# Kernel tuning notes

Hardware: AMD Instinct MI355X
Metric: run time of the kernel (lower is better)

Reference implementation:

```python
import jax, jax.numpy as jnp
import numpy as np

H = 12
DK = 64


def setup_inputs() -> dict:
    key = jax.random.key(0)
    ks = jax.random.split(key, 6)
    bs, ne, d = 32, 20, H * DK
    R = jax.random.normal(ks[0], (bs, ne, ne, d), dtype=jnp.float32)
    R_mas = jax.random.randint(ks[1], (bs, ne, ne, 1), 0, 2).astype(jnp.float32)
    WQ_w = jax.random.normal(ks[2], (DK, DK), dtype=jnp.float32) * (1.0 / np.sqrt(DK))
    WK_w = jax.random.normal(ks[3], (DK, DK), dtype=jnp.float32) * (1.0 / np.sqrt(DK))
    WV_w = jax.random.normal(ks[4], (DK, DK), dtype=jnp.float32) * (1.0 / np.sqrt(DK))
    zb = jnp.zeros((DK,), dtype=jnp.float32)
    return {"R": R, "R_mas": R_mas, "WQ_w": WQ_w, "WQ_b": zb, "WK_w": WK_w,
            "WK_b": zb, "WV_w": WV_w, "WV_b": zb}


def reference(R, R_mas, WQ_w, WQ_b, WK_w, WK_b, WV_w, WV_b):
    bs, ne, _, d = R.shape
    h, dk = H, DK
    n = ne * ne
    # (bs, h, ne, ne, dk)
    Rh = R.reshape(bs, ne, ne, h, dk).transpose(0, 3, 1, 2, 4)
    # per-head QKV linears (torch Linear: y = x @ W.T + b)
    Q = (Rh @ WQ_w.T + WQ_b).reshape(bs, h, n, dk)
    K = (Rh @ WK_w.T + WK_b).reshape(bs, h, n, dk)
    V = (Rh @ WV_w.T + WV_b).reshape(bs, h, n, dk)
    mas = R_mas.reshape(bs, 1, n)                      # (bs,1,n)
    att_mas = mas[:, :, :, None] * mas[:, :, None, :]  # (bs,1,n,n)
    alpha = jnp.einsum('bhqd,bhkd->bhqk', Q, K)        # (bs,h,n,n)
    alpha = alpha - (1.0 - att_mas) * 100000.0         # mask BEFORE scaling (faithful)
    alpha = jax.nn.softmax(alpha / jnp.sqrt(jnp.float32(dk)), axis=-1)
    R_Z = jnp.einsum('bhqk,bhkd->bhqd', alpha, V).reshape(bs, h, ne, ne, dk)
    R_Z = R_Z * R_mas.reshape(bs, 1, ne, ne, 1)
    # (bs, ne, ne, h*dk)
    return R_Z.transpose(0, 2, 3, 1, 4).reshape(bs, ne, ne, h * dk)
```

## Files before the change

### kernel.cpp

```cpp
#include <hip/hip_runtime.h>

typedef float    f32x4 __attribute__((ext_vector_type(4)));
typedef _Float16 f16x8 __attribute__((ext_vector_type(8)));
typedef _Float16 f16x4 __attribute__((ext_vector_type(4)));
typedef _Float16 f16x2 __attribute__((ext_vector_type(2)));
typedef __fp16   fp16x2_raw __attribute__((ext_vector_type(2)));

#define MFMA16 __builtin_amdgcn_mfma_f32_16x16x32_f16

__device__ __forceinline__ f16x2 pkrtz(float a, float b) {
    fp16x2_raw t = __builtin_amdgcn_cvt_pkrtz(a, b);
    union { fp16x2_raw r; f16x2 h; } u;
    u.r = t;
    return u.h;
}
#define PKRTZ pkrtz

#define NQ     400
#define DMODEL 768

#define SCL 0.18033688011112042f
#define PEN 18033.688011112043f
#define M0  8.0f

#define K_OFF    0
#define VT_OFF   51200
#define W_OFF    105472
#define PEN_OFF  130048
#define BIAS_OFF 131648
#define MKB_OFF  132416
#define SMEM_BYTES 132480

__device__ __forceinline__ f16x8 cvt8(const float* rp) {
    f32x4 u0 = *(const f32x4*)(rp);
    f32x4 u1 = *(const f32x4*)(rp + 4);
    union { f16x2 h2[4]; f16x8 v; } u;
    u.h2[0] = PKRTZ(u0[0], u0[1]);
    u.h2[1] = PKRTZ(u0[2], u0[3]);
    u.h2[2] = PKRTZ(u1[0], u1[1]);
    u.h2[3] = PKRTZ(u1[2], u1[3]);
    return u.v;
}

__device__ __forceinline__ void proj_v(char* smem, f16x8 af0, f16x8 af1,
                                       int t, int g, int q16, int csw) {
    #pragma unroll
    for (int cg = 0; cg < 4; ++cg) {
        const int col = cg * 16 + q16;
        const float bb = *(const float*)(smem + BIAS_OFF + (128 + col) * 4);
        f32x4 acc = {bb, bb, bb, bb};
        f16x8 wb0 = *(const f16x8*)(smem + W_OFF + 16384 + col * 128 + ((g * 16) ^ csw));
        f16x8 wb1 = *(const f16x8*)(smem + W_OFF + 16384 + col * 128 + ((64 + g * 16) ^ csw));
        acc = MFMA16(af0, wb0, acc, 0, 0, 0);
        acc = MFMA16(af1, wb1, acc, 0, 0, 0);
        union { f16x2 h2[2]; f16x4 v; } hv;
        hv.h2[0] = PKRTZ(acc[0], acc[1]);
        hv.h2[1] = PKRTZ(acc[2], acc[3]);
        *(f16x4*)(smem + VT_OFF + col * 848 + (t >> 1) * 64 + g * 16 + (t & 1) * 8) = hv.v;
    }
}

__device__ __forceinline__ void proj_k(char* smem, f16x8 af0, f16x8 af1,
                                       int kk, int g, int q16, int csw) {
    #pragma unroll
    for (int cg = 0; cg < 4; ++cg) {
        const int d0 = cg * 16 + 4 * g;
        f32x4 acc = *(const f32x4*)(smem + BIAS_OFF + (64 + d0) * 4);
        f16x8 wb0 = *(const f16x8*)(smem + W_OFF + 8192 + (cg * 16 + q16) * 128 + ((g * 16) ^ csw));
        f16x8 wb1 = *(const f16x8*)(smem + W_OFF + 8192 + (cg * 16 + q16) * 128 + ((64 + g * 16) ^ csw));
        acc = MFMA16(wb0, af0, acc, 0, 0, 0);
        acc = MFMA16(wb1, af1, acc, 0, 0, 0);
        union { f16x2 h2[2]; f16x4 v; } hv;
        hv.h2[0] = PKRTZ(acc[0], acc[1]);
        hv.h2[1] = PKRTZ(acc[2], acc[3]);
        const int pos2 = ((cg & 2) << 5) + g * 16 + (cg & 1) * 8;
        *(f16x4*)(smem + K_OFF + kk * 128 + (pos2 ^ csw)) = hv.v;
    }
}

__device__ __forceinline__ void proj_q(char* smem, f16x8 af0, f16x8 af1,
                                       int g, int q16, int csw, f16x8 (&qreg)[2]) {
    f32x4 qa[4];
    #pragma unroll
    for (int cg = 0; cg < 4; ++cg) {
        const int d0 = cg * 16 + 4 * g;
        f32x4 acc = *(const f32x4*)(smem + BIAS_OFF + d0 * 4);
        f16x8 wb0 = *(const f16x8*)(smem + W_OFF + (cg * 16 + q16) * 128 + ((g * 16) ^ csw));
        f16x8 wb1 = *(const f16x8*)(smem + W_OFF + (cg * 16 + q16) * 128 + ((64 + g * 16) ^ csw));
        acc = MFMA16(wb0, af0, acc, 0, 0, 0);
        acc = MFMA16(wb1, af1, acc, 0, 0, 0);
        qa[cg] = acc;
    }
    union { f16x2 h2[4]; f16x8 v; } u0, u1;
    u0.h2[0] = PKRTZ(qa[0][0], qa[0][1]);
    u0.h2[1] = PKRTZ(qa[0][2], qa[0][3]);
    u0.h2[2] = PKRTZ(qa[1][0], qa[1][1]);
    u0.h2[3] = PKRTZ(qa[1][2], qa[1][3]);
    u1.h2[0] = PKRTZ(qa[2][0], qa[2][1]);
    u1.h2[1] = PKRTZ(qa[2][2], qa[2][3]);
    u1.h2[2] = PKRTZ(qa[3][0], qa[3][1]);
    u1.h2[3] = PKRTZ(qa[3][2], qa[3][3]);
    qreg[0] = u0.v;
    qreg[1] = u1.v;
}

__global__ __launch_bounds__(1024, 4)
void attn_fused(const float* __restrict__ R, const float* __restrict__ Rmas,
                const float* __restrict__ Wq, const float* __restrict__ bq,
                const float* __restrict__ Wk, const float* __restrict__ bk,
                const float* __restrict__ Wv, const float* __restrict__ bv,
                float* __restrict__ out)
{
    extern __shared__ char smem[];
    const int tid  = threadIdx.x;
    const int lane = tid & 63;
    const int wv   = tid >> 6;
    const int g    = lane >> 4;
    const int q16  = lane & 15;
    const int csw  = (q16 & 7) << 4;

    const int blk = blockIdx.x;
    const int b   = blk / 12;
    const int h   = blk % 12;

    {
        if (tid < 768) {
            const int m   = tid >> 8;
            const int idx = tid & 255;
            const int row = idx >> 2;
            const int c0  = (idx & 3) << 4;
            const float* Wm = (m == 0 ? Wq : (m == 1 ? Wk : Wv)) + row * 64 + c0;
            const int sw = (row & 7) << 4;
            #pragma unroll
            for (int k2 = 0; k2 < 2; ++k2) {
                f32x4 v0 = *(const f32x4*)(Wm + 8 * k2);
                f32x4 v1 = *(const f32x4*)(Wm + 8 * k2 + 4);
                union { f16x2 h2[4]; f16x8 v; } hv;
                hv.h2[0] = PKRTZ(v0[0], v0[1]);
                hv.h2[1] = PKRTZ(v0[2], v0[3]);
                hv.h2[2] = PKRTZ(v1[0], v1[1]);
                hv.h2[3] = PKRTZ(v1[2], v1[3]);
                *(f16x8*)(smem + W_OFF + m * 8192 + row * 128 + ((c0 * 2 + 16 * k2) ^ sw)) = hv.v;
            }
        } else if (tid < 960) {
            const int jj = tid - 768;
            const float* bms[3] = {bq, bk, bv};
            *(float*)(smem + BIAS_OFF + jj * 4) = bms[jj >> 6][jj & 63];
        }
        if (wv < 7) {
            const int i = (wv << 6) | lane;
            const float mval = (i < NQ) ? Rmas[b * NQ + i] : 0.0f;
            unsigned long long bb = __ballot(mval != 0.0f);
            if (lane == 0) {
                ((unsigned*)(smem + MKB_OFF))[2 * wv]     = (unsigned)bb;
                ((unsigned*)(smem + MKB_OFF))[2 * wv + 1] = (unsigned)(bb >> 32);
            }
        }
        if (tid >= 512 && tid < 912) {
            const int k = tid - 512;
            *(float*)(smem + PEN_OFF + k * 4) =
                (Rmas[b * NQ + k] != 0.0f) ? -M0 : -(M0 + PEN);
        }
        if (tid < 256) {
            const int r = tid >> 2, c = tid & 3;
            *(f16x4*)(smem + VT_OFF + r * 848 + 768 + c * 16 + 8) = (f16x4){0, 0, 0, 0};
        }
    }
    __syncthreads();

    const float* Rbh = R + (size_t)b * NQ * DMODEL + h * 64;

    f16x8 qreg0[2], qreg1[2];
    const int qt0 = (2 * wv < 25)     ? (2 * wv)     : -1;
    const int qt1 = (2 * wv + 1 < 25) ? (2 * wv + 1) : -1;
    if (qt0 >= 0) {
        const float* rp = Rbh + (size_t)(qt0 * 16 + q16) * DMODEL + g * 8;
        f16x8 af0 = cvt8(rp);
        f16x8 af1 = cvt8(rp + 32);
        proj_k(smem, af0, af1, qt0 * 16 + q16, g, q16, csw);
        proj_v(smem, af0, af1, qt0, g, q16, csw);
        proj_q(smem, af0, af1, g, q16, csw, qreg0);
    }
    if (qt1 >= 0) {
        const float* rp = Rbh + (size_t)(qt1 * 16 + q16) * DMODEL + g * 8;
        f16x8 af0 = cvt8(rp);
        f16x8 af1 = cvt8(rp + 32);
        proj_k(smem, af0, af1, qt1 * 16 + q16, g, q16, csw);
        proj_v(smem, af0, af1, qt1, g, q16, csw);
        proj_q(smem, af0, af1, g, q16, csw, qreg1);
    }
    __syncthreads();

    if (qt0 >= 0) {
        const bool has2 = (qt1 >= 0);
        const int qrow0 = qt0 * 16 + q16;
        const unsigned qb0 = (((const unsigned*)(smem + MKB_OFF))[qrow0 >> 5] >> (qrow0 & 31)) & 1u;
        const int qrow1 = (has2 ? qt1 : qt0) * 16 + q16;
        const unsigned qb1 = (((const unsigned*)(smem + MKB_OFF))[qrow1 >> 5] >> (qrow1 & 31)) & 1u;

        const int kbase = K_OFF + q16 * 128;
        const int o0 = (g * 16) ^ csw;
        const int o1 = (64 + g * 16) ^ csw;

        f32x4 oc0[4], oc1[4];
        #pragma unroll
        for (int cg = 0; cg < 4; ++cg) {
            oc0[cg] = (f32x4){0.f, 0.f, 0.f, 0.f};
            oc1[cg] = (f32x4){0.f, 0.f, 0.f, 0.f};
        }
        float ps0 = 0.f, ps1 = 0.f;

        f16x8 ka0 = *(const f16x8*)(smem + kbase + o0);
        f16x8 ka1 = *(const f16x8*)(smem + kbase + o1);
        f16x8 kb0 = *(const f16x8*)(smem + kbase + 2048 + o0);
        f16x8 kb1 = *(const f16x8*)(smem + kbase + 2048 + o1);

        #pragma unroll 1
        for (int kc = 0; kc < 12; ++kc) {
            f32x4 pa4 = *(const f32x4*)(smem + PEN_OFF + (kc * 32 + 4 * g) * 4);
            f32x4 pb4 = *(const f32x4*)(smem + PEN_OFF + (kc * 32 + 16 + 4 * g) * 4);

            __builtin_amdgcn_s_setprio(1);
            f32x4 accA0 = {0.f, 0.f, 0.f, 0.f};
            accA0 = MFMA16(ka0, qreg0[0], accA0, 0, 0, 0);
            accA0 = MFMA16(ka1, qreg0[1], accA0, 0, 0, 0);
            f32x4 accB0 = {0.f, 0.f, 0.f, 0.f};
            accB0 = MFMA16(kb0, qreg0[0], accB0, 0, 0, 0);
            accB0 = MFMA16(kb1, qreg0[1], accB0, 0, 0, 0);
            f32x4 accA1 = {0.f, 0.f, 0.f, 0.f};
            f32x4 accB1 = {0.f, 0.f, 0.f, 0.f};
            if (has2) {
                accA1 = MFMA16(ka0, qreg1[0], accA1, 0, 0, 0);
                accA1 = MFMA16(ka1, qreg1[1], accA1, 0, 0, 0);
                accB1 = MFMA16(kb0, qreg1[0], accB1, 0, 0, 0);
                accB1 = MFMA16(kb1, qreg1[1], accB1, 0, 0, 0);
            }
            __builtin_amdgcn_s_setprio(0);

            const char* kn = smem + kbase + (kc + 1) * 4096;
            ka0 = *(const f16x8*)(kn + o0);
            ka1 = *(const f16x8*)(kn + o1);
            kb0 = *(const f16x8*)(kn + 2048 + o0);
            kb1 = *(const f16x8*)(kn + 2048 + o1);

            const float e0 = __builtin_amdgcn_exp2f(fmaf(accA0[0], SCL, pa4[0]));
            const float e1 = __builtin_amdgcn_exp2f(fmaf(accA0[1], SCL, pa4[1]));
            const float e2 = __builtin_amdgcn_exp2f(fmaf(accA0[2], SCL, pa4[2]));
            const float e3 = __builtin_amdgcn_exp2f(fmaf(accA0[3], SCL, pa4[3]));
            const float e4 = __builtin_amdgcn_exp2f(fmaf(accB0[0], SCL, pb4[0]));
            const float e5 = __builtin_amdgcn_exp2f(fmaf(accB0[1], SCL, pb4[1]));
            const float e6 = __builtin_amdgcn_exp2f(fmaf(accB0[2], SCL, pb4[2]));
            const float e7 = __builtin_amdgcn_exp2f(fmaf(accB0[3], SCL, pb4[3]));
            ps0 += ((e0 + e1) + (e2 + e3)) + ((e4 + e5) + (e6 + e7));
            union { f16x2 h2[4]; f16x8 v; } pu0;
            pu0.h2[0] = PKRTZ(e0, e1);
            pu0.h2[1] = PKRTZ(e2, e3);
            pu0.h2[2] = PKRTZ(e4, e5);
            pu0.h2[3] = PKRTZ(e6, e7);
            const f16x8 pfrag0 = pu0.v;

            f16x8 pfrag1;
            if (has2) {
                const float f0 = __builtin_amdgcn_exp2f(fmaf(accA1[0], SCL, pa4[0]));
                const float f1 = __builtin_amdgcn_exp2f(fmaf(accA1[1], SCL, pa4[1]));
                const float f2 = __builtin_amdgcn_exp2f(fmaf(accA1[2], SCL, pa4[2]));
                const float f3 = __builtin_amdgcn_exp2f(fmaf(accA1[3], SCL, pa4[3]));
                const float f4 = __builtin_amdgcn_exp2f(fmaf(accB1[0], SCL, pb4[0]));
                const float f5 = __builtin_amdgcn_exp2f(fmaf(accB1[1], SCL, pb4[1]));
                const float f6 = __builtin_amdgcn_exp2f(fmaf(accB1[2], SCL, pb4[2]));
                const float f7 = __builtin_amdgcn_exp2f(fmaf(accB1[3], SCL, pb4[3]));
                ps1 += ((f0 + f1) + (f2 + f3)) + ((f4 + f5) + (f6 + f7));
                union { f16x2 h2[4]; f16x8 v; } pu1;
                pu1.h2[0] = PKRTZ(f0, f1);
                pu1.h2[1] = PKRTZ(f2, f3);
                pu1.h2[2] = PKRTZ(f4, f5);
                pu1.h2[3] = PKRTZ(f6, f7);
                pfrag1 = pu1.v;
            }

            __builtin_amdgcn_s_setprio(1);
            #pragma unroll
            for (int cg = 0; cg < 4; ++cg) {
                f16x8 vb = *(const f16x8*)(smem + VT_OFF + (cg * 16 + q16) * 848 + kc * 64 + g * 16);
                oc0[cg] = MFMA16(pfrag0, vb, oc0[cg], 0, 0, 0);
                if (has2) oc1[cg] = MFMA16(pfrag1, vb, oc1[cg], 0, 0, 0);
            }
            __builtin_amdgcn_s_setprio(0);
        }
        {
            f32x4 pa4 = *(const f32x4*)(smem + PEN_OFF + (384 + 4 * g) * 4);
            f32x4 accA0 = {0.f, 0.f, 0.f, 0.f};
            accA0 = MFMA16(ka0, qreg0[0], accA0, 0, 0, 0);
            accA0 = MFMA16(ka1, qreg0[1], accA0, 0, 0, 0);
            const float e0 = __builtin_amdgcn_exp2f(fmaf(accA0[0], SCL, pa4[0]));
            const float e1 = __builtin_amdgcn_exp2f(fmaf(accA0[1], SCL, pa4[1]));
            const float e2 = __builtin_amdgcn_exp2f(fmaf(accA0[2], SCL, pa4[2]));
            const float e3 = __builtin_amdgcn_exp2f(fmaf(accA0[3], SCL, pa4[3]));
            ps0 += (e0 + e1) + (e2 + e3);
            union { f16x2 h2[4]; f16x8 v; } pu0;
            pu0.h2[0] = PKRTZ(e0, e1);
            pu0.h2[1] = PKRTZ(e2, e3);
            pu0.h2[2] = (f16x2){0, 0};
            pu0.h2[3] = (f16x2){0, 0};
            const f16x8 pfrag0 = pu0.v;

            f16x8 pfrag1;
            if (has2) {
                f32x4 accA1 = {0.f, 0.f, 0.f, 0.f};
                accA1 = MFMA16(ka0, qreg1[0], accA1, 0, 0, 0);
                accA1 = MFMA16(ka1, qreg1[1], accA1, 0, 0, 0);
                const float f0 = __builtin_amdgcn_exp2f(fmaf(accA1[0], SCL, pa4[0]));
                const float f1 = __builtin_amdgcn_exp2f(fmaf(accA1[1], SCL, pa4[1]));
                const float f2 = __builtin_amdgcn_exp2f(fmaf(accA1[2], SCL, pa4[2]));
                const float f3 = __builtin_amdgcn_exp2f(fmaf(accA1[3], SCL, pa4[3]));
                ps1 += (f0 + f1) + (f2 + f3);
                union { f16x2 h2[4]; f16x8 v; } pu1;
                pu1.h2[0] = PKRTZ(f0, f1);
                pu1.h2[1] = PKRTZ(f2, f3);
                pu1.h2[2] = (f16x2){0, 0};
                pu1.h2[3] = (f16x2){0, 0};
                pfrag1 = pu1.v;
            }
            #pragma unroll
            for (int cg = 0; cg < 4; ++cg) {
                f16x8 vb = *(const f16x8*)(smem + VT_OFF + (cg * 16 + q16) * 848 + 12 * 64 + g * 16);
                oc0[cg] = MFMA16(pfrag0, vb, oc0[cg], 0, 0, 0);
                if (has2) oc1[cg] = MFMA16(pfrag1, vb, oc1[cg], 0, 0, 0);
            }
        }

        ps0 += __shfl_xor(ps0, 16);
        ps0 += __shfl_xor(ps0, 32);
        const float myrs0 = qb0 ? __builtin_amdgcn_rcpf(ps0) : 0.0f;
        float rs[4];
        #pragma unroll
        for (int r = 0; r < 4; ++r) rs[r] = __shfl(myrs0, 4 * g + r);
        float* op0 = out + (size_t)(b * NQ + qt0 * 16) * DMODEL + h * 64;
        #pragma unroll
        for (int r = 0; r < 4; ++r) {
            #pragma unroll
            for (int cg = 0; cg < 4; ++cg)
                op0[(4 * g + r) * DMODEL + cg * 16 + q16] = oc0[cg][r] * rs[r];
        }
        if (has2) {
            ps1 += __shfl_xor(ps1, 16);
            ps1 += __shfl_xor(ps1, 32);
            const float myrs1 = qb1 ? __builtin_amdgcn_rcpf(ps1) : 0.0f;
            #pragma unroll
            for (int r = 0; r < 4; ++r) rs[r] = __shfl(myrs1, 4 * g + r);
            float* op1 = out + (size_t)(b * NQ + qt1 * 16) * DMODEL + h * 64;
            #pragma unroll
            for (int r = 0; r < 4; ++r) {
                #pragma unroll
                for (int cg = 0; cg < 4; ++cg)
                    op1[(4 * g + r) * DMODEL + cg * 16 + q16] = oc1[cg][r] * rs[r];
            }
        }
    }
}

extern "C" void kernel_launch(void* const* d_in, const int* in_sizes, int n_in,
                              void* d_out, int out_size, void* d_ws, size_t ws_size,
                              hipStream_t stream) {
    const float* R    = (const float*)d_in[0];
    const float* Rmas = (const float*)d_in[1];
    const float* Wq   = (const float*)d_in[2];
    const float* bq   = (const float*)d_in[3];
    const float* Wk   = (const float*)d_in[4];
    const float* bk   = (const float*)d_in[5];
    const float* Wv   = (const float*)d_in[6];
    const float* bv   = (const float*)d_in[7];
    float* out = (float*)d_out;

    (void)hipFuncSetAttribute(reinterpret_cast<const void*>(attn_fused),
                              hipFuncAttributeMaxDynamicSharedMemorySize, SMEM_BYTES);
    attn_fused<<<dim3(384), dim3(1024), SMEM_BYTES, stream>>>(R, Rmas, Wq, bq, Wk, bk, Wv, bv, out);
}
```

Measured before the change: 41.18 us.

## Split work into 1.5 heads per block to match 256-CU grid

The grid goes from 384 blocks (one per batch-head) to 256 blocks. Each block now processes one full head plus half of another head's query tiles, so the work spreads evenly across the 256 compute units and there is no partial second wave. The per-head body moves into a noinline device function that is called twice with a barrier between the calls. Both calls recompute the full K/V projection, so half-head segments repeat K/V work, and the noinline call may add register and call overhead.

Result: slower. 50.51 us (+22.7%).

```diff
diff --git a/kernel.cpp b/kernel.cpp
--- a/kernel.cpp
+++ b/kernel.cpp
@@ -104,92 +104,35 @@
     qreg[1] = u1.v;
 }
 
-__global__ __launch_bounds__(1024, 4)
-void attn_fused(const float* __restrict__ R, const float* __restrict__ Rmas,
-                const float* __restrict__ Wq, const float* __restrict__ bq,
-                const float* __restrict__ Wk, const float* __restrict__ bk,
-                const float* __restrict__ Wv, const float* __restrict__ bv,
-                float* __restrict__ out)
-{
-    extern __shared__ char smem[];
-    const int tid  = threadIdx.x;
-    const int lane = tid & 63;
-    const int wv   = tid >> 6;
-    const int g    = lane >> 4;
-    const int q16  = lane & 15;
-    const int csw  = (q16 & 7) << 4;
-
-    const int blk = blockIdx.x;
-    const int b   = blk / 12;
-    const int h   = blk % 12;
-
-    {
-        if (tid < 768) {
-            const int m   = tid >> 8;
-            const int idx = tid & 255;
-            const int row = idx >> 2;
-            const int c0  = (idx & 3) << 4;
-            const float* Wm = (m == 0 ? Wq : (m == 1 ? Wk : Wv)) + row * 64 + c0;
-            const int sw = (row & 7) << 4;
-            #pragma unroll
-            for (int k2 = 0; k2 < 2; ++k2) {
-                f32x4 v0 = *(const f32x4*)(Wm + 8 * k2);
-                f32x4 v1 = *(const f32x4*)(Wm + 8 * k2 + 4);
-                union { f16x2 h2[4]; f16x8 v; } hv;
-                hv.h2[0] = PKRTZ(v0[0], v0[1]);
-                hv.h2[1] = PKRTZ(v0[2], v0[3]);
-                hv.h2[2] = PKRTZ(v1[0], v1[1]);
-                hv.h2[3] = PKRTZ(v1[2], v1[3]);
-                *(f16x8*)(smem + W_OFF + m * 8192 + row * 128 + ((c0 * 2 + 16 * k2) ^ sw)) = hv.v;
-            }
-        } else if (tid < 960) {
-            const int jj = tid - 768;
-            const float* bms[3] = {bq, bk, bv};
-            *(float*)(smem + BIAS_OFF + jj * 4) = bms[jj >> 6][jj & 63];
-        }
-        if (wv < 7) {
-            const int i = (wv << 6) | lane;
-            const float mval = (i < NQ) ? Rmas[b * NQ + i] : 0.0f;
-            unsigned long long bb = __ballot(mval != 0.0f);
-            if (lane == 0) {
-                ((unsigned*)(smem + MKB_OFF))[2 * wv]     = (unsigned)bb;
-                ((unsigned*)(smem + MKB_OFF))[2 * wv + 1] = (unsigned)(bb >> 32);
-            }
-        }
-        if (tid >= 512 && tid < 912) {
-            const int k = tid - 512;
-            *(float*)(smem + PEN_OFF + k * 4) =
-                (Rmas[b * NQ + k] != 0.0f) ? -M0 : -(M0 + PEN);
-        }
-        if (tid < 256) {
-            const int r = tid >> 2, c = tid & 3;
-            *(f16x4*)(smem + VT_OFF + r * 848 + 768 + c * 16 + 8) = (f16x4){0, 0, 0, 0};
-        }
-    }
-    __syncthreads();
-
-    const float* Rbh = R + (size_t)b * NQ * DMODEL + h * 64;
-
+__attribute__((noinline)) __device__
+void run_seg(char* smem, const float* __restrict__ Rbh, float* __restrict__ outh,
+             int qlo, int qhi, int wv, int g, int q16, int csw) {
+    const int tA = 2 * wv, tB = 2 * wv + 1;
+    const bool own0 = (tA >= qlo) && (tA < qhi);
+    const bool own1 = (tB >= qlo) && (tB < qhi);
     f16x8 qreg0[2], qreg1[2];
-    const int qt0 = (2 * wv < 25)     ? (2 * wv)     : -1;
-    const int qt1 = (2 * wv + 1 < 25) ? (2 * wv + 1) : -1;
-    if (qt0 >= 0) {
-        const float* rp = Rbh + (size_t)(qt0 * 16 + q16) * DMODEL + g * 8;
+
+    if (tA < 25) {
+        const float* rp = Rbh + (size_t)(tA * 16 + q16) * DMODEL + g * 8;
         f16x8 af0 = cvt8(rp);
         f16x8 af1 = cvt8(rp + 32);
-        proj_k(smem, af0, af1, qt0 * 16 + q16, g, q16, csw);
-        proj_v(smem, af0, af1, qt0, g, q16, csw);
-        proj_q(smem, af0, af1, g, q16, csw, qreg0);
-    }
-    if (qt1 >= 0) {
-        const float* rp = Rbh + (size_t)(qt1 * 16 + q16) * DMODEL + g * 8;
+        proj_k(smem, af0, af1, tA * 16 + q16, g, q16, csw);
+        proj_v(smem, af0, af1, tA, g, q16, csw);
+        if (own0) proj_q(smem, af0, af1, g, q16, csw, qreg0);
+    }
+    if (tB < 25) {
+        const float* rp = Rbh + (size_t)(tB * 16 + q16) * DMODEL + g * 8;
         f16x8 af0 = cvt8(rp);
         f16x8 af1 = cvt8(rp + 32);
-        proj_k(smem, af0, af1, qt1 * 16 + q16, g, q16, csw);
-        proj_v(smem, af0, af1, qt1, g, q16, csw);
-        proj_q(smem, af0, af1, g, q16, csw, qreg1);
+        proj_k(smem, af0, af1, tB * 16 + q16, g, q16, csw);
+        proj_v(smem, af0, af1, tB, g, q16, csw);
+        if (own1) proj_q(smem, af0, af1, g, q16, csw, qreg1);
     }
     __syncthreads();
+
+    int qt0 = own0 ? tA : (own1 ? tB : -1);
+    const int qt1 = (own0 && own1) ? tB : -1;
+    if (!own0 && own1) { qreg0[0] = qreg1[0]; qreg0[1] = qreg1[1]; }
 
     if (qt0 >= 0) {
         const bool has2 = (qt1 >= 0);
@@ -335,7 +278,7 @@
         float rs[4];
         #pragma unroll
         for (int r = 0; r < 4; ++r) rs[r] = __shfl(myrs0, 4 * g + r);
-        float* op0 = out + (size_t)(b * NQ + qt0 * 16) * DMODEL + h * 64;
+        float* op0 = outh + (size_t)(qt0 * 16) * DMODEL;
         #pragma unroll
         for (int r = 0; r < 4; ++r) {
             #pragma unroll
@@ -348,7 +291,7 @@
             const float myrs1 = qb1 ? __builtin_amdgcn_rcpf(ps1) : 0.0f;
             #pragma unroll
             for (int r = 0; r < 4; ++r) rs[r] = __shfl(myrs1, 4 * g + r);
-            float* op1 = out + (size_t)(b * NQ + qt1 * 16) * DMODEL + h * 64;
+            float* op1 = outh + (size_t)(qt1 * 16) * DMODEL;
             #pragma unroll
             for (int r = 0; r < 4; ++r) {
                 #pragma unroll
@@ -357,6 +300,81 @@
             }
         }
     }
+}
+
+__global__ __launch_bounds__(1024, 4)
+void attn_fused(const float* __restrict__ R, const float* __restrict__ Rmas,
+                const float* __restrict__ Wq, const float* __restrict__ bq,
+                const float* __restrict__ Wk, const float* __restrict__ bk,
+                const float* __restrict__ Wv, const float* __restrict__ bv,
+                float* __restrict__ out)
+{
+    extern __shared__ char smem[];
+    const int tid  = threadIdx.x;
+    const int lane = tid & 63;
+    const int wv   = tid >> 6;
+    const int g    = lane >> 4;
+    const int q16  = lane & 15;
+    const int csw  = (q16 & 7) << 4;
+
+    const int blk = blockIdx.x;
+    const int b   = blk >> 3;
+    const int j   = blk & 7;
+    int h_full, h_half, qlo2, qhi2;
+    if (j & 1) { h_half = (3 * j - 1) >> 1; qlo2 = 13; qhi2 = 25; h_full = (3 * j + 1) >> 1; }
+    else       { h_full = (3 * j) >> 1;     h_half = h_full + 1; qlo2 = 0;  qhi2 = 13; }
+
+    {
+        if (tid < 768) {
+            const int m   = tid >> 8;
+            const int idx = tid & 255;
+            const int row = idx >> 2;
+            const int c0  = (idx & 3) << 4;
+            const float* Wm = (m == 0 ? Wq : (m == 1 ? Wk : Wv)) + row * 64 + c0;
+            const int sw = (row & 7) << 4;
+            #pragma unroll
+            for (int k2 = 0; k2 < 2; ++k2) {
+                f32x4 v0 = *(const f32x4*)(Wm + 8 * k2);
+                f32x4 v1 = *(const f32x4*)(Wm + 8 * k2 + 4);
+                union { f16x2 h2[4]; f16x8 v; } hv;
+                hv.h2[0] = PKRTZ(v0[0], v0[1]);
+                hv.h2[1] = PKRTZ(v0[2], v0[3]);
+                hv.h2[2] = PKRTZ(v1[0], v1[1]);
+                hv.h2[3] = PKRTZ(v1[2], v1[3]);
+                *(f16x8*)(smem + W_OFF + m * 8192 + row * 128 + ((c0 * 2 + 16 * k2) ^ sw)) = hv.v;
+            }
+        } else if (tid < 960) {
+            const int jj = tid - 768;
+            const float* bms[3] = {bq, bk, bv};
+            *(float*)(smem + BIAS_OFF + jj * 4) = bms[jj >> 6][jj & 63];
+        }
+        if (wv < 7) {
+            const int i = (wv << 6) | lane;
+            const float mval = (i < NQ) ? Rmas[b * NQ + i] : 0.0f;
+            unsigned long long bb = __ballot(mval != 0.0f);
+            if (lane == 0) {
+                ((unsigned*)(smem + MKB_OFF))[2 * wv]     = (unsigned)bb;
+                ((unsigned*)(smem + MKB_OFF))[2 * wv + 1] = (unsigned)(bb >> 32);
+            }
+        }
+        if (tid >= 512 && tid < 912) {
+            const int k = tid - 512;
+            *(float*)(smem + PEN_OFF + k * 4) =
+                (Rmas[b * NQ + k] != 0.0f) ? -M0 : -(M0 + PEN);
+        }
+        if (tid < 256) {
+            const int r = tid >> 2, c = tid & 3;
+            *(f16x4*)(smem + VT_OFF + r * 848 + 768 + c * 16 + 8) = (f16x4){0, 0, 0, 0};
+        }
+    }
+    __syncthreads();
+
+    const float* Rb = R + (size_t)b * NQ * DMODEL;
+    float* outb = out + (size_t)b * NQ * DMODEL;
+
+    run_seg(smem, Rb + h_full * 64, outb + h_full * 64, 0, 25, wv, g, q16, csw);
+    __syncthreads();
+    run_seg(smem, Rb + h_half * 64, outb + h_half * 64, qlo2, qhi2, wv, g, q16, csw);
 }
 
 extern "C" void kernel_launch(void* const* d_in, const int* in_sizes, int n_in,
@@ -374,5 +392,5 @@
 
     (void)hipFuncSetAttribute(reinterpret_cast<const void*>(attn_fused),
                               hipFuncAttributeMaxDynamicSharedMemorySize, SMEM_BYTES);
-    attn_fused<<<dim3(384), dim3(1024), SMEM_BYTES, stream>>>(R, Rmas, Wq, bq, Wk, bk, Wv, bv, out);
-}
+    attn_fused<<<dim3(256), dim3(1024), SMEM_BYTES, stream>>>(R, Rmas, Wq, bq, Wk, bk, Wv, bv, out);
+}
```
